# Performance work log

Measured on AMD Instinct MI355X. Metric: run time of the kernel, lower is better.

Reference implementation:

```python
import jax, jax.numpy as jnp
import numpy as np

B, S, MW = 128, 256, 21          # batch, sentence length, max word length
VOCAB, E_CHAR, E_WORD, K = 100, 50, 256, 5


def setup_inputs() -> dict:
    key = jax.random.key(0)
    ks = jax.random.split(key, 6)
    padded_sents = jax.random.randint(ks[0], (B, S, MW), 0, VOCAB)
    emb_table = jax.random.normal(ks[1], (VOCAB, E_CHAR), jnp.float32) * 0.1
    emb_table = emb_table.at[0].set(0.0)  # pad_token_idx row zeroed (padding_idx)
    conv_w = jax.random.normal(ks[2], (E_WORD, E_CHAR, K), jnp.float32) * 0.05
    conv_b = jnp.zeros((E_WORD,), jnp.float32)
    w_proj = jax.random.normal(ks[3], (E_WORD, E_WORD), jnp.float32) * 0.05
    b_proj = jnp.zeros((E_WORD,), jnp.float32)
    w_gate = jax.random.normal(ks[4], (E_WORD, E_WORD), jnp.float32) * 0.05
    b_gate = jnp.zeros((E_WORD,), jnp.float32)
    return {
        "padded_sents": padded_sents,
        "emb_table": emb_table,
        "conv_w": conv_w,
        "conv_b": conv_b,
        "w_proj": w_proj,
        "b_proj": b_proj,
        "w_gate": w_gate,
        "b_gate": b_gate,
    }


def reference(padded_sents, emb_table, conv_w, conv_b, w_proj, b_proj, w_gate, b_gate):
    b, s, mw = padded_sents.shape
    # char embedding lookup: [B,S,MW,E_CHAR]
    x = emb_table[padded_sents]
    # fold (B,S) into one batch dim and move channels first: [B*S, E_CHAR, MW]
    x = x.reshape(b * s, mw, -1).transpose(0, 2, 1)
    # Conv1d VALID over char positions: [B*S, E_WORD, MW-K+1]
    y = jax.lax.conv_general_dilated(
        x, conv_w, window_strides=(1,), padding="VALID",
        dimension_numbers=("NCH", "OIH", "NCH"))
    y = jax.nn.relu(y + conv_b[None, :, None])
    # max-pool over remaining char positions: [B*S, E_WORD]
    y = jnp.max(y, axis=2)
    # Highway network
    proj = jax.nn.relu(y @ w_proj.T + b_proj)
    gate = jax.nn.sigmoid(y @ w_gate.T + b_gate)
    out = gate * proj + (1.0 - gate) * y
    # dropout in eval mode (identity)
    return out.reshape(b, s, -1)
```

## Files before the change

kernel.cpp:

```cpp
#include <hip/hip_runtime.h>

#define B_     128
#define S_     256
#define MW_    21
#define VOCAB_ 100
#define EC_    50
#define EW_    256
#define KW_    5
#define T_     17
#define NW_    (B_ * S_)
#define GROWS  (VOCAB_ * KW_)
#define WPB    128
#define P1B    200

typedef _Float16 f16x8 __attribute__((ext_vector_type(8)));
typedef float    f32x4 __attribute__((ext_vector_type(4)));

__global__ __launch_bounds__(256) void k_prep(const float* __restrict__ emb,
                                              const float* __restrict__ cw,
                                              const float* __restrict__ Wp,
                                              const float* __restrict__ Wg,
                                              _Float16* __restrict__ g,
                                              _Float16* __restrict__ wpf,
                                              _Float16* __restrict__ wgf) {
  const int bi = blockIdx.x;
  if (bi < P1B) {
    __shared__ float ls[64 * 250];
    const int vp = bi >> 2, ot = bi & 3;
    const int o0 = ot * 64;
    const int tid = threadIdx.x;
    const float4* __restrict__ cw4 = (const float4*)cw + ot * 4000;
#pragma unroll 4
    for (int idx4 = tid; idx4 < 4000; idx4 += 256)
      *(float4*)&ls[idx4 * 4] = cw4[idx4];
    __syncthreads();

    const int l = tid & 63, wv = tid >> 6;
#pragma unroll
    for (int vv = 0; vv < 2; ++vv) {
      const int v = vp * 2 + vv;
      const float* __restrict__ er = emb + v * EC_;
      float acc = 0.f;
#pragma unroll
      for (int i = 0; i < EC_; ++i)
        acc += er[i] * ls[l * 250 + i * KW_ + wv];
      g[(v * KW_ + wv) * EW_ + o0 + l] = (_Float16)acc;
      if (wv == 0) {
        float a4 = 0.f;
#pragma unroll
        for (int i = 0; i < EC_; ++i)
          a4 += er[i] * ls[l * 250 + i * KW_ + 4];
        g[(v * KW_ + 4) * EW_ + o0 + l] = (_Float16)a4;
      }
    }
  } else {
    const int fl  = (bi - P1B) * 256 + threadIdx.x;
    const int nt  = fl >> 9;
    const int rem = fl & 511;
    const int ks  = rem >> 6;
    const int l   = rem & 63;
    const int n   = nt * 16 + (l & 15);
    const int kc  = ks * 32 + (l >> 4) * 8;
    const int src = n * EW_ + kc;
    const float4 p0 = *(const float4*)&Wp[src], p1 = *(const float4*)&Wp[src + 4];
    const float4 q0 = *(const float4*)&Wg[src], q1 = *(const float4*)&Wg[src + 4];
    f16x8 hp = {(_Float16)p0.x, (_Float16)p0.y, (_Float16)p0.z, (_Float16)p0.w,
                (_Float16)p1.x, (_Float16)p1.y, (_Float16)p1.z, (_Float16)p1.w};
    f16x8 hg = {(_Float16)q0.x, (_Float16)q0.y, (_Float16)q0.z, (_Float16)q0.w,
                (_Float16)q1.x, (_Float16)q1.y, (_Float16)q1.z, (_Float16)q1.w};
    *(f16x8*)&wpf[fl * 8] = hp;
    *(f16x8*)&wgf[fl * 8] = hg;
  }
}

__global__ __launch_bounds__(512, 2) void k_mega(const int* __restrict__ idx,
                                                 const _Float16* __restrict__ g,
                                                 const float* __restrict__ cb,
                                                 const _Float16* __restrict__ wpf,
                                                 const _Float16* __restrict__ wgf,
                                                 const float* __restrict__ bp,
                                                 const float* __restrict__ bg,
                                                 float* __restrict__ out) {
  __shared__ __align__(16) _Float16 lds[32768 + GROWS * 64];
  _Float16* y_s = lds;
  _Float16* g_s = lds + 32768;

  const int tid  = threadIdx.x;
  const int wave = tid >> 6, lane = tid & 63;
  const int m0 = blockIdx.x * WPB;
  const int wq = lane >> 3, og = lane & 7;

#pragma unroll
  for (int i = 0; i < 8; ++i) {
    const int c = tid + i * 512;
    if (c < GROWS * 8) {
      const int row = c >> 3, cc = c & 7;
      const int sl = cc ^ ((row / 5) & 7);
      *(f16x8*)&g_s[row * 64 + sl * 8] = *(const f16x8*)&g[row * EW_ + cc * 8];
    }
  }
  __syncthreads();

  f16x8 pre[8];
#pragma unroll
  for (int chunk = 0; chunk < 4; ++chunk) {
    const int oc0 = chunk * 64;
    if (chunk < 3) {
#pragma unroll
      for (int i = 0; i < 8; ++i) {
        const int c = tid + i * 512;
        if (c < GROWS * 8) {
          const int row = c >> 3, cc = c & 7;
          pre[i] = *(const f16x8*)&g[row * EW_ + oc0 + 64 + cc * 8];
        }
      }
    }

    f16x8 bias;
#pragma unroll
    for (int j = 0; j < 8; ++j) bias[j] = (_Float16)cb[oc0 + og * 8 + j];

    const int ks_w    = chunk * 2 + (og >> 2);
    const int lane_hi = (og & 3) << 4;

#pragma unroll
    for (int it = 0; it < 2; ++it) {
      const int wl = it * 64 + wave * 8 + wq;
      const int* __restrict__ ip = idx + (m0 + wl) * MW_;
      int base[MW_];
#pragma unroll
      for (int c = 0; c < MW_; ++c) {
        const int ipc = ip[c];
        base[c] = ipc * (KW_ * 64) + ((og ^ (ipc & 7)) << 3);
      }

      const _Float16 NEG = (_Float16)(-60000.0f);
      f16x8 mx = {NEG, NEG, NEG, NEG, NEG, NEG, NEG, NEG};
#pragma unroll
      for (int t = 0; t < T_; ++t) {
        f16x8 s = *(const f16x8*)&g_s[base[t]];
#pragma unroll
        for (int k = 1; k < KW_; ++k)
          s += *(const f16x8*)&g_s[base[t + k] + k * 64];
        mx = __builtin_elementwise_max(mx, s);
      }
      const f16x8 zero8 = {0, 0, 0, 0, 0, 0, 0, 0};
      mx = __builtin_elementwise_max(mx + bias, zero8);

      const int mt = wl >> 4;
      const int lt = ((wl & 15) | lane_hi) ^ og;
      *(f16x8*)&y_s[((mt * 8 + ks_w) * 64 + lt) * 8] = mx;
    }
    __syncthreads();
    if (chunk < 3) {
#pragma unroll
      for (int i = 0; i < 8; ++i) {
        const int c = tid + i * 512;
        if (c < GROWS * 8) {
          const int row = c >> 3, cc = c & 7;
          const int sl = cc ^ ((row / 5) & 7);
          *(f16x8*)&g_s[row * 64 + sl * 8] = pre[i];
        }
      }
      __syncthreads();
    }
  }

  const int mtp = wave >> 1, nh = wave & 1;
  const int quad = lane >> 4, r16 = lane & 15;

  f16x8 a[2][8];
#pragma unroll
  for (int mi = 0; mi < 2; ++mi)
#pragma unroll
    for (int ks = 0; ks < 8; ++ks) {
      const int key = ((ks & 1) << 2) | quad;
      a[mi][ks] = *(const f16x8*)&y_s[(((mtp * 2 + mi) * 8 + ks) * 64 + (lane ^ key)) * 8];
    }

  const f32x4 zero = {0.f, 0.f, 0.f, 0.f};
#pragma unroll
  for (int h = 0; h < 2; ++h) {
    f32x4 accp[2][4], accg[2][4];
#pragma unroll
    for (int mi = 0; mi < 2; ++mi)
#pragma unroll
      for (int nf = 0; nf < 4; ++nf) { accp[mi][nf] = zero; accg[mi][nf] = zero; }

#pragma unroll
    for (int nf = 0; nf < 4; ++nf) {
      const int nt = h * 8 + nh * 4 + nf;
#pragma unroll
      for (int ks = 0; ks < 8; ++ks) {
        const int off = ((nt * 8 + ks) * 64 + lane) * 8;
        const f16x8 bpv = *(const f16x8*)&wpf[off];
        const f16x8 bgv = *(const f16x8*)&wgf[off];
#pragma unroll
        for (int mi = 0; mi < 2; ++mi) {
          accp[mi][nf] = __builtin_amdgcn_mfma_f32_16x16x32_f16(a[mi][ks], bpv, accp[mi][nf], 0, 0, 0);
          accg[mi][nf] = __builtin_amdgcn_mfma_f32_16x16x32_f16(a[mi][ks], bgv, accg[mi][nf], 0, 0, 0);
        }
      }
    }

#pragma unroll
    for (int mi = 0; mi < 2; ++mi) {
      const int mt = mtp * 2 + mi;
#pragma unroll
      for (int nf = 0; nf < 4; ++nf) {
        const int n = h * 128 + nh * 64 + nf * 16 + r16;
        const float bpn = bp[n];
        const float bgn = bg[n];
        const int ks_e = n >> 5;
        const int lane_e = ((n >> 3) & 3) << 4;
        const int og_e = (n >> 3) & 7;
        const int je = n & 7;
#pragma unroll
        for (int reg = 0; reg < 4; ++reg) {
          const int m = mt * 16 + quad * 4 + reg;
          float p = fmaxf(accp[mi][nf][reg] + bpn, 0.f);
          const float gz = accg[mi][nf][reg] + bgn;
          const float gate = 1.f / (1.f + __expf(-gz));
          const float yv =
              (float)y_s[((mt * 8 + ks_e) * 64 + (((m & 15) | lane_e) ^ og_e)) * 8 + je];
          out[(m0 + m) * EW_ + n] = gate * p + (1.f - gate) * yv;
        }
      }
    }
  }
}

extern "C" void kernel_launch(void* const* d_in, const int* in_sizes, int n_in,
                              void* d_out, int out_size, void* d_ws, size_t ws_size,
                              hipStream_t stream) {
  (void)in_sizes; (void)n_in; (void)out_size; (void)ws_size;
  const int*   idx = (const int*)d_in[0];
  const float* emb = (const float*)d_in[1];
  const float* cw  = (const float*)d_in[2];
  const float* cb  = (const float*)d_in[3];
  const float* wp  = (const float*)d_in[4];
  const float* bpp = (const float*)d_in[5];
  const float* wgt = (const float*)d_in[6];
  const float* bgg = (const float*)d_in[7];
  float* out = (float*)d_out;
  _Float16* g_ws = (_Float16*)d_ws;
  _Float16* wp_f = g_ws + GROWS * EW_;
  _Float16* wg_f = wp_f + EW_ * EW_;

  k_prep<<<P1B + 32, 256, 0, stream>>>(emb, cw, wp, wgt, g_ws, wp_f, wg_f);
  k_mega<<<NW_ / WPB, 512, 0, stream>>>(idx, g_ws, cb, wp_f, wg_f, bpp, bgg, out);
}
```

Before: 124.5 us.

## Use 1024-thread blocks with one word per thread-group and drop g_s swizzle

Doubles the block size to 1024 threads so each group of 8 lanes handles a single word instead of two. The char indices and base offsets are now loaded once and hoisted out of the chunk loop. Each wave now owns one 16-row M tile in the highway GEMM instead of two, which roughly halves accumulator register pressure per thread. The XOR swizzle on the gathered table in LDS is removed, which makes addressing simpler but risks more LDS bank conflicts. Each wave also reloads the weight fragments for its smaller M tile, raising global/L2 traffic per output.

New measurement: 137.0 us. 10.0% more time.

```diff
diff --git a/kernel.cpp b/kernel.cpp
--- a/kernel.cpp
+++ b/kernel.cpp
@@ -73,14 +73,14 @@
   }
 }
 
-__global__ __launch_bounds__(512, 2) void k_mega(const int* __restrict__ idx,
-                                                 const _Float16* __restrict__ g,
-                                                 const float* __restrict__ cb,
-                                                 const _Float16* __restrict__ wpf,
-                                                 const _Float16* __restrict__ wgf,
-                                                 const float* __restrict__ bp,
-                                                 const float* __restrict__ bg,
-                                                 float* __restrict__ out) {
+__global__ __launch_bounds__(1024, 4) void k_mega(const int* __restrict__ idx,
+                                                  const _Float16* __restrict__ g,
+                                                  const float* __restrict__ cb,
+                                                  const _Float16* __restrict__ wpf,
+                                                  const _Float16* __restrict__ wgf,
+                                                  const float* __restrict__ bp,
+                                                  const float* __restrict__ bg,
+                                                  float* __restrict__ out) {
   __shared__ __align__(16) _Float16 lds[32768 + GROWS * 64];
   _Float16* y_s = lds;
   _Float16* g_s = lds + 32768;
@@ -91,24 +91,35 @@
   const int wq = lane >> 3, og = lane & 7;
 
 #pragma unroll
-  for (int i = 0; i < 8; ++i) {
-    const int c = tid + i * 512;
+  for (int i = 0; i < 4; ++i) {
+    const int c = tid + i * 1024;
     if (c < GROWS * 8) {
       const int row = c >> 3, cc = c & 7;
-      const int sl = cc ^ ((row / 5) & 7);
-      *(f16x8*)&g_s[row * 64 + sl * 8] = *(const f16x8*)&g[row * EW_ + cc * 8];
+      *(f16x8*)&g_s[row * 64 + cc * 8] = *(const f16x8*)&g[row * EW_ + cc * 8];
     }
   }
   __syncthreads();
 
-  f16x8 pre[8];
+  const int wl = wave * 8 + wq;
+  const int* __restrict__ ipr = idx + (m0 + wl) * MW_;
+  int base[MW_];
+#pragma unroll
+  for (int c = 0; c < MW_; ++c)
+    base[c] = ipr[c] * (KW_ * 64) + og * 8;
+  const int mt_a   = wl >> 4;
+  const int lt_lo  = wl & 15;
+  const int ks_hi  = og >> 2;
+  const int lane_hi = (og & 3) << 4;
+  const int lt = (lt_lo | lane_hi) ^ og;
+
+  f16x8 pre[4];
 #pragma unroll
   for (int chunk = 0; chunk < 4; ++chunk) {
     const int oc0 = chunk * 64;
     if (chunk < 3) {
 #pragma unroll
-      for (int i = 0; i < 8; ++i) {
-        const int c = tid + i * 512;
+      for (int i = 0; i < 4; ++i) {
+        const int c = tid + i * 1024;
         if (c < GROWS * 8) {
           const int row = c >> 3, cc = c & 7;
           pre[i] = *(const f16x8*)&g[row * EW_ + oc0 + 64 + cc * 8];
@@ -120,46 +131,29 @@
 #pragma unroll
     for (int j = 0; j < 8; ++j) bias[j] = (_Float16)cb[oc0 + og * 8 + j];
 
-    const int ks_w    = chunk * 2 + (og >> 2);
-    const int lane_hi = (og & 3) << 4;
-
-#pragma unroll
-    for (int it = 0; it < 2; ++it) {
-      const int wl = it * 64 + wave * 8 + wq;
-      const int* __restrict__ ip = idx + (m0 + wl) * MW_;
-      int base[MW_];
-#pragma unroll
-      for (int c = 0; c < MW_; ++c) {
-        const int ipc = ip[c];
-        base[c] = ipc * (KW_ * 64) + ((og ^ (ipc & 7)) << 3);
-      }
-
-      const _Float16 NEG = (_Float16)(-60000.0f);
-      f16x8 mx = {NEG, NEG, NEG, NEG, NEG, NEG, NEG, NEG};
-#pragma unroll
-      for (int t = 0; t < T_; ++t) {
-        f16x8 s = *(const f16x8*)&g_s[base[t]];
-#pragma unroll
-        for (int k = 1; k < KW_; ++k)
-          s += *(const f16x8*)&g_s[base[t + k] + k * 64];
-        mx = __builtin_elementwise_max(mx, s);
-      }
-      const f16x8 zero8 = {0, 0, 0, 0, 0, 0, 0, 0};
-      mx = __builtin_elementwise_max(mx + bias, zero8);
-
-      const int mt = wl >> 4;
-      const int lt = ((wl & 15) | lane_hi) ^ og;
-      *(f16x8*)&y_s[((mt * 8 + ks_w) * 64 + lt) * 8] = mx;
-    }
+    const _Float16 NEG = (_Float16)(-60000.0f);
+    f16x8 mx = {NEG, NEG, NEG, NEG, NEG, NEG, NEG, NEG};
+#pragma unroll
+    for (int t = 0; t < T_; ++t) {
+      f16x8 s = *(const f16x8*)&g_s[base[t]];
+#pragma unroll
+      for (int k = 1; k < KW_; ++k)
+        s += *(const f16x8*)&g_s[base[t + k] + k * 64];
+      mx = __builtin_elementwise_max(mx, s);
+    }
+    const f16x8 zero8 = {0, 0, 0, 0, 0, 0, 0, 0};
+    mx = __builtin_elementwise_max(mx + bias, zero8);
+
+    *(f16x8*)&y_s[((mt_a * 8 + (chunk * 2 + ks_hi)) * 64 + lt) * 8] = mx;
+
     __syncthreads();
     if (chunk < 3) {
 #pragma unroll
-      for (int i = 0; i < 8; ++i) {
-        const int c = tid + i * 512;
+      for (int i = 0; i < 4; ++i) {
+        const int c = tid + i * 1024;
         if (c < GROWS * 8) {
           const int row = c >> 3, cc = c & 7;
-          const int sl = cc ^ ((row / 5) & 7);
-          *(f16x8*)&g_s[row * 64 + sl * 8] = pre[i];
+          *(f16x8*)&g_s[row * 64 + cc * 8] = pre[i];
         }
       }
       __syncthreads();
@@ -169,23 +163,19 @@
   const int mtp = wave >> 1, nh = wave & 1;
   const int quad = lane >> 4, r16 = lane & 15;
 
-  f16x8 a[2][8];
-#pragma unroll
-  for (int mi = 0; mi < 2; ++mi)
-#pragma unroll
-    for (int ks = 0; ks < 8; ++ks) {
-      const int key = ((ks & 1) << 2) | quad;
-      a[mi][ks] = *(const f16x8*)&y_s[(((mtp * 2 + mi) * 8 + ks) * 64 + (lane ^ key)) * 8];
-    }
+  f16x8 a[8];
+#pragma unroll
+  for (int ks = 0; ks < 8; ++ks) {
+    const int key = ((ks & 1) << 2) | quad;
+    a[ks] = *(const f16x8*)&y_s[((mtp * 8 + ks) * 64 + (lane ^ key)) * 8];
+  }
 
   const f32x4 zero = {0.f, 0.f, 0.f, 0.f};
 #pragma unroll
   for (int h = 0; h < 2; ++h) {
-    f32x4 accp[2][4], accg[2][4];
-#pragma unroll
-    for (int mi = 0; mi < 2; ++mi)
-#pragma unroll
-      for (int nf = 0; nf < 4; ++nf) { accp[mi][nf] = zero; accg[mi][nf] = zero; }
+    f32x4 accp[4], accg[4];
+#pragma unroll
+    for (int nf = 0; nf < 4; ++nf) { accp[nf] = zero; accg[nf] = zero; }
 
 #pragma unroll
     for (int nf = 0; nf < 4; ++nf) {
@@ -195,36 +185,29 @@
         const int off = ((nt * 8 + ks) * 64 + lane) * 8;
         const f16x8 bpv = *(const f16x8*)&wpf[off];
         const f16x8 bgv = *(const f16x8*)&wgf[off];
-#pragma unroll
-        for (int mi = 0; mi < 2; ++mi) {
-          accp[mi][nf] = __builtin_amdgcn_mfma_f32_16x16x32_f16(a[mi][ks], bpv, accp[mi][nf], 0, 0, 0);
-          accg[mi][nf] = __builtin_amdgcn_mfma_f32_16x16x32_f16(a[mi][ks], bgv, accg[mi][nf], 0, 0, 0);
-        }
-      }
-    }
-
-#pragma unroll
-    for (int mi = 0; mi < 2; ++mi) {
-      const int mt = mtp * 2 + mi;
-#pragma unroll
-      for (int nf = 0; nf < 4; ++nf) {
-        const int n = h * 128 + nh * 64 + nf * 16 + r16;
-        const float bpn = bp[n];
-        const float bgn = bg[n];
-        const int ks_e = n >> 5;
-        const int lane_e = ((n >> 3) & 3) << 4;
-        const int og_e = (n >> 3) & 7;
-        const int je = n & 7;
-#pragma unroll
-        for (int reg = 0; reg < 4; ++reg) {
-          const int m = mt * 16 + quad * 4 + reg;
-          float p = fmaxf(accp[mi][nf][reg] + bpn, 0.f);
-          const float gz = accg[mi][nf][reg] + bgn;
-          const float gate = 1.f / (1.f + __expf(-gz));
-          const float yv =
-              (float)y_s[((mt * 8 + ks_e) * 64 + (((m & 15) | lane_e) ^ og_e)) * 8 + je];
-          out[(m0 + m) * EW_ + n] = gate * p + (1.f - gate) * yv;
-        }
+        accp[nf] = __builtin_amdgcn_mfma_f32_16x16x32_f16(a[ks], bpv, accp[nf], 0, 0, 0);
+        accg[nf] = __builtin_amdgcn_mfma_f32_16x16x32_f16(a[ks], bgv, accg[nf], 0, 0, 0);
+      }
+    }
+
+#pragma unroll
+    for (int nf = 0; nf < 4; ++nf) {
+      const int n = h * 128 + nh * 64 + nf * 16 + r16;
+      const float bpn = bp[n];
+      const float bgn = bg[n];
+      const int ks_e = n >> 5;
+      const int lane_e = ((n >> 3) & 3) << 4;
+      const int og_e = (n >> 3) & 7;
+      const int je = n & 7;
+#pragma unroll
+      for (int reg = 0; reg < 4; ++reg) {
+        const int m = mtp * 16 + quad * 4 + reg;
+        float p = fmaxf(accp[nf][reg] + bpn, 0.f);
+        const float gz = accg[nf][reg] + bgn;
+        const float gate = 1.f / (1.f + __expf(-gz));
+        const float yv =
+            (float)y_s[((mtp * 8 + ks_e) * 64 + (((m & 15) | lane_e) ^ og_e)) * 8 + je];
+        out[(m0 + m) * EW_ + n] = gate * p + (1.f - gate) * yv;
       }
     }
   }
@@ -248,5 +231,5 @@
   _Float16* wg_f = wp_f + EW_ * EW_;
 
   k_prep<<<P1B + 32, 256, 0, stream>>>(emb, cw, wp, wgt, g_ws, wp_f, wg_f);
-  k_mega<<<NW_ / WPB, 512, 0, stream>>>(idx, g_ws, cb, wp_f, wg_f, bpp, bgg, out);
+  k_mega<<<NW_ / WPB, 1024, 0, stream>>>(idx, g_ws, cb, wp_f, wg_f, bpp, bgg, out);
 }
```

## Interleave projection GEMM with conv chunks and drop g_s LDS swizzle

Applied to the files above, without the earlier changes.

Starts accumulating the projection-branch MFMAs for each K-slice as soon as its conv chunk is written to LDS, so matrix work overlaps with the gather/max phase instead of running entirely afterwards. The gate-branch GEMM stays in the epilogue. It also removes the XOR swizzle on the gathered conv table in LDS, which simplifies address math but may bring back bank conflicts on the random-index gathers. The projection accumulators now stay live for the whole kernel, which raises register pressure at 512 threads with two blocks per CU.

New measurement: 124.2 us. Within noise of the previous version (-0.3%).

```diff
diff --git a/kernel.cpp b/kernel.cpp
--- a/kernel.cpp
+++ b/kernel.cpp
@@ -90,16 +90,25 @@
   const int m0 = blockIdx.x * WPB;
   const int wq = lane >> 3, og = lane & 7;
 
+  const int mtp = wave >> 1, nh = wave & 1;
+  const int quad = lane >> 4, r16 = lane & 15;
+
 #pragma unroll
   for (int i = 0; i < 8; ++i) {
     const int c = tid + i * 512;
     if (c < GROWS * 8) {
       const int row = c >> 3, cc = c & 7;
-      const int sl = cc ^ ((row / 5) & 7);
-      *(f16x8*)&g_s[row * 64 + sl * 8] = *(const f16x8*)&g[row * EW_ + cc * 8];
+      *(f16x8*)&g_s[row * 64 + cc * 8] = *(const f16x8*)&g[row * EW_ + cc * 8];
     }
   }
   __syncthreads();
+
+  const f32x4 zero = {0.f, 0.f, 0.f, 0.f};
+  f32x4 accp[2][8];
+#pragma unroll
+  for (int mi = 0; mi < 2; ++mi)
+#pragma unroll
+    for (int o = 0; o < 8; ++o) accp[mi][o] = zero;
 
   f16x8 pre[8];
 #pragma unroll
@@ -129,10 +138,8 @@
       const int* __restrict__ ip = idx + (m0 + wl) * MW_;
       int base[MW_];
 #pragma unroll
-      for (int c = 0; c < MW_; ++c) {
-        const int ipc = ip[c];
-        base[c] = ipc * (KW_ * 64) + ((og ^ (ipc & 7)) << 3);
-      }
+      for (int c = 0; c < MW_; ++c)
+        base[c] = ip[c] * (KW_ * 64) + og * 8;
 
       const _Float16 NEG = (_Float16)(-60000.0f);
       f16x8 mx = {NEG, NEG, NEG, NEG, NEG, NEG, NEG, NEG};
@@ -158,16 +165,29 @@
         const int c = tid + i * 512;
         if (c < GROWS * 8) {
           const int row = c >> 3, cc = c & 7;
-          const int sl = cc ^ ((row / 5) & 7);
-          *(f16x8*)&g_s[row * 64 + sl * 8] = pre[i];
+          *(f16x8*)&g_s[row * 64 + cc * 8] = pre[i];
         }
       }
       __syncthreads();
     }
-  }
-
-  const int mtp = wave >> 1, nh = wave & 1;
-  const int quad = lane >> 4, r16 = lane & 15;
+
+#pragma unroll
+    for (int ks2 = 0; ks2 < 2; ++ks2) {
+      const int ks = chunk * 2 + ks2;
+      const int key = ((ks & 1) << 2) | quad;
+      const f16x8 a0 =
+          *(const f16x8*)&y_s[(((mtp * 2 + 0) * 8 + ks) * 64 + (lane ^ key)) * 8];
+      const f16x8 a1 =
+          *(const f16x8*)&y_s[(((mtp * 2 + 1) * 8 + ks) * 64 + (lane ^ key)) * 8];
+#pragma unroll
+      for (int o = 0; o < 8; ++o) {
+        const int nt = (o >> 2) * 8 + nh * 4 + (o & 3);
+        const f16x8 bpv = *(const f16x8*)&wpf[((nt * 8 + ks) * 64 + lane) * 8];
+        accp[0][o] = __builtin_amdgcn_mfma_f32_16x16x32_f16(a0, bpv, accp[0][o], 0, 0, 0);
+        accp[1][o] = __builtin_amdgcn_mfma_f32_16x16x32_f16(a1, bpv, accp[1][o], 0, 0, 0);
+      }
+    }
+  }
 
   f16x8 a[2][8];
 #pragma unroll
@@ -178,14 +198,13 @@
       a[mi][ks] = *(const f16x8*)&y_s[(((mtp * 2 + mi) * 8 + ks) * 64 + (lane ^ key)) * 8];
     }
 
-  const f32x4 zero = {0.f, 0.f, 0.f, 0.f};
 #pragma unroll
   for (int h = 0; h < 2; ++h) {
-    f32x4 accp[2][4], accg[2][4];
+    f32x4 accg[2][4];
 #pragma unroll
     for (int mi = 0; mi < 2; ++mi)
 #pragma unroll
-      for (int nf = 0; nf < 4; ++nf) { accp[mi][nf] = zero; accg[mi][nf] = zero; }
+      for (int nf = 0; nf < 4; ++nf) accg[mi][nf] = zero;
 
 #pragma unroll
     for (int nf = 0; nf < 4; ++nf) {
@@ -193,13 +212,10 @@
 #pragma unroll
       for (int ks = 0; ks < 8; ++ks) {
         const int off = ((nt * 8 + ks) * 64 + lane) * 8;
-        const f16x8 bpv = *(const f16x8*)&wpf[off];
         const f16x8 bgv = *(const f16x8*)&wgf[off];
 #pragma unroll
-        for (int mi = 0; mi < 2; ++mi) {
-          accp[mi][nf] = __builtin_amdgcn_mfma_f32_16x16x32_f16(a[mi][ks], bpv, accp[mi][nf], 0, 0, 0);
+        for (int mi = 0; mi < 2; ++mi)
           accg[mi][nf] = __builtin_amdgcn_mfma_f32_16x16x32_f16(a[mi][ks], bgv, accg[mi][nf], 0, 0, 0);
-        }
       }
     }
 
@@ -218,7 +234,7 @@
 #pragma unroll
         for (int reg = 0; reg < 4; ++reg) {
           const int m = mt * 16 + quad * 4 + reg;
-          float p = fmaxf(accp[mi][nf][reg] + bpn, 0.f);
+          float p = fmaxf(accp[mi][h * 4 + nf][reg] + bpn, 0.f);
           const float gz = accg[mi][nf][reg] + bgn;
           const float gate = 1.f / (1.f + __expf(-gz));
           const float yv =
```

## Retile highway GEMM to 4x4 wave tiles and drop g_s swizzle

Applied to the files above, without the earlier changes.

The highway GEMM wave tiling changes from 2 M-tiles by 8 N-tiles (two passes) to 4 M-tiles by 4 N-tiles in a single pass. Each weight fragment loaded from global memory now feeds four MFMAs instead of two, roughly halving global weight traffic per wave. The cost is holding 32 f32x4 accumulators at once, which raises register pressure under launch_bounds(512,2). Separately, the XOR swizzle on the g_s conv table is removed, which simplifies address math but may bring back LDS bank conflicts on the gather reads.

After: 120.3 us. 1.03x faster.

```diff
diff --git a/kernel.cpp b/kernel.cpp
--- a/kernel.cpp
+++ b/kernel.cpp
@@ -95,8 +95,7 @@
     const int c = tid + i * 512;
     if (c < GROWS * 8) {
       const int row = c >> 3, cc = c & 7;
-      const int sl = cc ^ ((row / 5) & 7);
-      *(f16x8*)&g_s[row * 64 + sl * 8] = *(const f16x8*)&g[row * EW_ + cc * 8];
+      *(f16x8*)&g_s[row * 64 + cc * 8] = *(const f16x8*)&g[row * EW_ + cc * 8];
     }
   }
   __syncthreads();
@@ -129,10 +128,8 @@
       const int* __restrict__ ip = idx + (m0 + wl) * MW_;
       int base[MW_];
 #pragma unroll
-      for (int c = 0; c < MW_; ++c) {
-        const int ipc = ip[c];
-        base[c] = ipc * (KW_ * 64) + ((og ^ (ipc & 7)) << 3);
-      }
+      for (int c = 0; c < MW_; ++c)
+        base[c] = ip[c] * (KW_ * 64) + og * 8;
 
       const _Float16 NEG = (_Float16)(-60000.0f);
       f16x8 mx = {NEG, NEG, NEG, NEG, NEG, NEG, NEG, NEG};
@@ -158,73 +155,65 @@
         const int c = tid + i * 512;
         if (c < GROWS * 8) {
           const int row = c >> 3, cc = c & 7;
-          const int sl = cc ^ ((row / 5) & 7);
-          *(f16x8*)&g_s[row * 64 + sl * 8] = pre[i];
+          *(f16x8*)&g_s[row * 64 + cc * 8] = pre[i];
         }
       }
       __syncthreads();
     }
   }
 
-  const int mtp = wave >> 1, nh = wave & 1;
+  const int mtp2 = wave >> 2, nq = wave & 3;
   const int quad = lane >> 4, r16 = lane & 15;
 
-  f16x8 a[2][8];
-#pragma unroll
-  for (int mi = 0; mi < 2; ++mi)
-#pragma unroll
-    for (int ks = 0; ks < 8; ++ks) {
-      const int key = ((ks & 1) << 2) | quad;
-      a[mi][ks] = *(const f16x8*)&y_s[(((mtp * 2 + mi) * 8 + ks) * 64 + (lane ^ key)) * 8];
-    }
-
   const f32x4 zero = {0.f, 0.f, 0.f, 0.f};
-#pragma unroll
-  for (int h = 0; h < 2; ++h) {
-    f32x4 accp[2][4], accg[2][4];
-#pragma unroll
-    for (int mi = 0; mi < 2; ++mi)
-#pragma unroll
-      for (int nf = 0; nf < 4; ++nf) { accp[mi][nf] = zero; accg[mi][nf] = zero; }
-
+  f32x4 accp[4][4], accg[4][4];
+#pragma unroll
+  for (int mi = 0; mi < 4; ++mi)
+#pragma unroll
+    for (int nf = 0; nf < 4; ++nf) { accp[mi][nf] = zero; accg[mi][nf] = zero; }
+
+#pragma unroll
+  for (int ks = 0; ks < 8; ++ks) {
+    const int key = ((ks & 1) << 2) | quad;
+    f16x8 a[4];
+#pragma unroll
+    for (int mi = 0; mi < 4; ++mi)
+      a[mi] = *(const f16x8*)&y_s[(((mtp2 * 4 + mi) * 8 + ks) * 64 + (lane ^ key)) * 8];
 #pragma unroll
     for (int nf = 0; nf < 4; ++nf) {
-      const int nt = h * 8 + nh * 4 + nf;
-#pragma unroll
-      for (int ks = 0; ks < 8; ++ks) {
-        const int off = ((nt * 8 + ks) * 64 + lane) * 8;
-        const f16x8 bpv = *(const f16x8*)&wpf[off];
-        const f16x8 bgv = *(const f16x8*)&wgf[off];
-#pragma unroll
-        for (int mi = 0; mi < 2; ++mi) {
-          accp[mi][nf] = __builtin_amdgcn_mfma_f32_16x16x32_f16(a[mi][ks], bpv, accp[mi][nf], 0, 0, 0);
-          accg[mi][nf] = __builtin_amdgcn_mfma_f32_16x16x32_f16(a[mi][ks], bgv, accg[mi][nf], 0, 0, 0);
-        }
-      }
-    }
-
-#pragma unroll
-    for (int mi = 0; mi < 2; ++mi) {
-      const int mt = mtp * 2 + mi;
-#pragma unroll
-      for (int nf = 0; nf < 4; ++nf) {
-        const int n = h * 128 + nh * 64 + nf * 16 + r16;
-        const float bpn = bp[n];
-        const float bgn = bg[n];
-        const int ks_e = n >> 5;
-        const int lane_e = ((n >> 3) & 3) << 4;
-        const int og_e = (n >> 3) & 7;
-        const int je = n & 7;
-#pragma unroll
-        for (int reg = 0; reg < 4; ++reg) {
-          const int m = mt * 16 + quad * 4 + reg;
-          float p = fmaxf(accp[mi][nf][reg] + bpn, 0.f);
-          const float gz = accg[mi][nf][reg] + bgn;
-          const float gate = 1.f / (1.f + __expf(-gz));
-          const float yv =
-              (float)y_s[((mt * 8 + ks_e) * 64 + (((m & 15) | lane_e) ^ og_e)) * 8 + je];
-          out[(m0 + m) * EW_ + n] = gate * p + (1.f - gate) * yv;
-        }
+      const int nt = nq * 4 + nf;
+      const int off = ((nt * 8 + ks) * 64 + lane) * 8;
+      const f16x8 bpv = *(const f16x8*)&wpf[off];
+      const f16x8 bgv = *(const f16x8*)&wgf[off];
+#pragma unroll
+      for (int mi = 0; mi < 4; ++mi) {
+        accp[mi][nf] = __builtin_amdgcn_mfma_f32_16x16x32_f16(a[mi], bpv, accp[mi][nf], 0, 0, 0);
+        accg[mi][nf] = __builtin_amdgcn_mfma_f32_16x16x32_f16(a[mi], bgv, accg[mi][nf], 0, 0, 0);
+      }
+    }
+  }
+
+#pragma unroll
+  for (int mi = 0; mi < 4; ++mi) {
+    const int mt = mtp2 * 4 + mi;
+#pragma unroll
+    for (int nf = 0; nf < 4; ++nf) {
+      const int n = nq * 64 + nf * 16 + r16;
+      const float bpn = bp[n];
+      const float bgn = bg[n];
+      const int ks_e = n >> 5;
+      const int lane_e = ((n >> 3) & 3) << 4;
+      const int og_e = (n >> 3) & 7;
+      const int je = n & 7;
+#pragma unroll
+      for (int reg = 0; reg < 4; ++reg) {
+        const int m = mt * 16 + quad * 4 + reg;
+        float p = fmaxf(accp[mi][nf][reg] + bpn, 0.f);
+        const float gz = accg[mi][nf][reg] + bgn;
+        const float gate = 1.f / (1.f + __expf(-gz));
+        const float yv =
+            (float)y_s[((mt * 8 + ks_e) * 64 + (((m & 15) | lane_e) ^ og_e)) * 8 + je];
+        out[(m0 + m) * EW_ + n] = gate * p + (1.f - gate) * yv;
       }
     }
   }
```
